# Kernel optimization log

Measured on AMD Instinct MI355X. Metric: run time of the kernel, lower is better.

Reference implementation:

```python
import jax, jax.numpy as jnp
import numpy as np

B, S, HID = 1, 2048, 4096
NH, NKV, HD = 32, 8, 128
GROUPS = NH // NKV
ROPE_THETA = 10000.0


def rotate_half(x):
    x1, x2 = jnp.split(x, 2, axis=-1)
    return jnp.concatenate([-x2, x1], axis=-1)


def rope_cos_sin(position_ids, head_dim, dtype):
    # inv_freq: [hd/2]; position_ids: [B, S]
    inv_freq = 1.0 / (ROPE_THETA ** (jnp.arange(0, head_dim, 2, dtype=jnp.float32) / head_dim))
    freqs = position_ids.astype(jnp.float32)[..., None] * inv_freq  # [B, S, hd/2]
    emb = jnp.concatenate([freqs, freqs], axis=-1)                  # [B, S, hd]
    return jnp.cos(emb).astype(dtype), jnp.sin(emb).astype(dtype)


def apply_rope(x, cos, sin):
    # x: [B, H, S, hd]; cos/sin: [B, S, hd] -> broadcast over heads
    return x * cos[:, None] + rotate_half(x) * sin[:, None]


def setup_inputs() -> dict:
    key = jax.random.key(0)
    ks = jax.random.split(key, 5)
    scale = 0.02
    return {
        "hidden_states": jax.random.normal(ks[0], (B, S, HID), dtype=jnp.float32),
        "wq": jax.random.normal(ks[1], (HID, NH * HD), dtype=jnp.float32) * scale,
        "wk": jax.random.normal(ks[2], (HID, NKV * HD), dtype=jnp.float32) * scale,
        "wv": jax.random.normal(ks[3], (HID, NKV * HD), dtype=jnp.float32) * scale,
        "wo": jax.random.normal(ks[4], (NH * HD, HID), dtype=jnp.float32) * scale,
        "position_ids": jnp.arange(S, dtype=jnp.int32)[None, :],
    }


def reference(hidden_states, wq, wk, wv, wo, position_ids):
    bsz, q_len, _ = hidden_states.shape
    # projections (nn.Linear, bias=False)
    q = (hidden_states @ wq).reshape(bsz, q_len, NH, HD).transpose(0, 2, 1, 3)   # [B,NH,S,hd]
    k = (hidden_states @ wk).reshape(bsz, q_len, NKV, HD).transpose(0, 2, 1, 3)  # [B,NKV,S,hd]
    v = (hidden_states @ wv).reshape(bsz, q_len, NKV, HD).transpose(0, 2, 1, 3)
    # RoPE applied to Q and K at global positions (prefill: no past cache)
    cos, sin = rope_cos_sin(position_ids, HD, q.dtype)
    q = apply_rope(q, cos, sin)
    k = apply_rope(k, cos, sin)
    # GQA: expand KV heads to query heads
    k_full = jnp.repeat(k, GROUPS, axis=1)  # [B,NH,S,hd]
    v_full = jnp.repeat(v, GROUPS, axis=1)
    # prefill flash attention == causal SDPA
    logits = jnp.einsum('bhqd,bhkd->bhqk', q, k_full) / jnp.sqrt(jnp.asarray(HD, q.dtype))
    causal = jnp.tril(jnp.ones((q_len, q_len), dtype=bool))
    neg = jnp.asarray(jnp.finfo(q.dtype).min, q.dtype)
    logits = jnp.where(causal[None, None], logits, neg)
    probs = jax.nn.softmax(logits, axis=-1)                     # [B,NH,S,S]
    attn = jnp.einsum('bhqk,bhkd->bhqd', probs, v_full)          # [B,NH,S,hd]
    attn_output = attn.transpose(0, 2, 1, 3).reshape(bsz, q_len, NH * HD) @ wo
    # chunked prefill eviction scores: causal attention probs accumulated over
    # all queries, aggregated per KV head group -> [B, NKV, kv_len]
    accumulated_scores = probs.sum(axis=2).reshape(bsz, NKV, GROUPS, q_len).sum(axis=2)
    return attn_output, accumulated_scores
```

## Files before the change

### kernel.cpp

```cpp
#include <hip/hip_runtime.h>
#include <hip/hip_bf16.h>
#include <cstdint>
#include <cstddef>

#define S_LEN 2048
#define HID_DIM 4096
#define NH 32
#define NKV 8
#define HD 128
#define LOG2E 1.4426950408889634f
#define SCALE 0.08838834764831845f

typedef __attribute__((ext_vector_type(8))) short bf16x8;
typedef __attribute__((ext_vector_type(4))) float f32x4;
typedef __attribute__((ext_vector_type(16))) float f32x16;
typedef __attribute__((ext_vector_type(4))) short short4v;
typedef __attribute__((ext_vector_type(4))) unsigned u32x4;

__device__ __forceinline__ short f2bf(float f) {
  union { float f; unsigned u; } v; v.f = f;
  return (short)((v.u + 0x7fffu + ((v.u >> 16) & 1u)) >> 16);
}
__device__ __forceinline__ float bf2f(short s) {
  union { unsigned u; float f; } v; v.u = ((unsigned)(unsigned short)s) << 16;
  return v.f;
}
__device__ __forceinline__ unsigned cvt_pk_bf16(float lo, float hi) {
  unsigned r;
  asm("v_cvt_pk_bf16_f32 %0, %1, %2" : "=v"(r) : "v"(lo), "v"(hi));
  return r;
}
__device__ __forceinline__ void gld_lds16(const void* g, void* l) {
  __builtin_amdgcn_global_load_lds((const __attribute__((address_space(1))) unsigned*)g,
                                   (__attribute__((address_space(3))) unsigned*)l, 16, 0, 0);
}

#define WAITVM8() asm volatile("s_waitcnt vmcnt(8)" ::: "memory")
#define WAITVM4() asm volatile("s_waitcnt vmcnt(4)" ::: "memory")
#define WAITVM0() asm volatile("s_waitcnt vmcnt(0)" ::: "memory")

__global__ void cvt_kernel(const float* __restrict__ in, short* __restrict__ out, int n) {
  int i = (blockIdx.x * 256 + threadIdx.x) * 4;
  if (i < n) {
    float4 f = *(const float4*)(in + i);
    short4v o = { f2bf(f.x), f2bf(f.y), f2bf(f.z), f2bf(f.w) };
    *(short4v*)(out + i) = o;
  }
}

__global__ void tconv_kernel(const float* __restrict__ in, short* __restrict__ out, int R, int C) {
  __shared__ float tile[32][33];
  int tr = blockIdx.y * 32, tc = blockIdx.x * 32;
  int tx = threadIdx.x & 31, ty = threadIdx.x >> 5;
#pragma unroll
  for (int i = 0; i < 32; i += 8)
    tile[ty + i][tx] = in[(size_t)(tr + ty + i) * C + tc + tx];
  __syncthreads();
#pragma unroll
  for (int i = 0; i < 32; i += 8)
    out[(size_t)(tc + ty + i) * R + tr + tx] = f2bf(tile[tx][ty + i]);
}

template<int MODE>
__global__ __launch_bounds__(256, 4) void gemm_bt_kernel(
    const short* __restrict__ A, const short* __restrict__ Bt,
    void* __restrict__ Cout, int M, int N, int K, int rchunk, int cchunk)
{
  __shared__ short As[2][128 * 32];
  __shared__ short Bs[2][128 * 32];
  const int tid = threadIdx.x;
  const int lane = tid & 63;
  const int w = tid >> 6;
  const int wm = w >> 1, wn = w & 1;
  const int xcd = blockIdx.x & 7;
  const int local = blockIdx.x >> 3;
  const int by = (xcd >> 2) * rchunk + (local % rchunk);
  const int bx = (xcd & 3) * cchunk + (local / rchunk);
  const int m0 = by * 128, n0 = bx * 128;

  auto stage = [&](int bb, int k0) {
#pragma unroll
    for (int rep = 0; rep < 2; rep++) {
      int c = rep * 256 + tid;
      int row = c >> 2, slot = c & 3;
      int gs = slot ^ (row & 3);
      gld_lds16(A + (size_t)(m0 + row) * K + k0 + gs * 8, &As[bb][c * 8]);
      gld_lds16(Bt + (size_t)(n0 + row) * K + k0 + gs * 8, &Bs[bb][c * 8]);
    }
  };

  f32x4 acc[4][4];
#pragma unroll
  for (int i = 0; i < 4; i++)
#pragma unroll
    for (int j = 0; j < 4; j++) acc[i][j] = (f32x4){0.f, 0.f, 0.f, 0.f};

  const int NT = K >> 5;
  stage(0, 0);
  for (int kt = 0; kt < NT; kt++) {
    const int b = kt & 1;
    if (kt + 1 < NT) { stage(b ^ 1, (kt + 1) << 5); WAITVM4(); }
    else             { WAITVM0(); }
    __builtin_amdgcn_s_barrier();

    bf16x8 af[4], bf[4];
#pragma unroll
    for (int ms = 0; ms < 4; ms++) {
      int row = wm * 64 + ms * 16 + (lane & 15);
      af[ms] = *(const bf16x8*)(&As[b][row * 32 + (((lane >> 4) ^ (row & 3)) << 3)]);
    }
#pragma unroll
    for (int ns = 0; ns < 4; ns++) {
      int row = wn * 64 + ns * 16 + (lane & 15);
      bf[ns] = *(const bf16x8*)(&Bs[b][row * 32 + (((lane >> 4) ^ (row & 3)) << 3)]);
    }
#pragma unroll
    for (int ms = 0; ms < 4; ms++)
#pragma unroll
      for (int ns = 0; ns < 4; ns++)
        acc[ms][ns] = __builtin_amdgcn_mfma_f32_16x16x32_bf16(af[ms], bf[ns], acc[ms][ns], 0, 0, 0);

    __builtin_amdgcn_s_barrier();
  }

#pragma unroll
  for (int ms = 0; ms < 4; ms++) {
    int mb = m0 + wm * 64 + ms * 16 + ((lane >> 4) << 2);
#pragma unroll
    for (int ns = 0; ns < 4; ns++) {
      int n = n0 + wn * 64 + ns * 16 + (lane & 15);
      if (MODE == 3) {
        short* o = (short*)Cout;
        if (n < NH * HD) {
          int head = n >> 7, d = n & 127;
#pragma unroll
          for (int r = 0; r < 4; r++)
            o[((size_t)head * M + (mb + r)) * HD + d] = f2bf(acc[ms][ns][r]);
        } else if (n < (NH + NKV) * HD) {
          int head = (n - NH * HD) >> 7, d = n & 127;
          short* ok = o + (size_t)NH * S_LEN * HD;
#pragma unroll
          for (int r = 0; r < 4; r++)
            ok[((size_t)head * M + (mb + r)) * HD + d] = f2bf(acc[ms][ns][r]);
        } else {
          int head = (n - (NH + NKV) * HD) >> 7, d = n & 127;
          short* ov = o + (size_t)(NH + NKV) * S_LEN * HD;
          short4v pk;
#pragma unroll
          for (int r = 0; r < 4; r++) pk[r] = f2bf(acc[ms][ns][r]);
          *(short4v*)(ov + ((size_t)head * HD + d) * M + mb) = pk;
        }
      } else {
        float* o = (float*)Cout;
#pragma unroll
        for (int r = 0; r < 4; r++)
          o[(size_t)(mb + r) * N + n] = acc[ms][ns][r];
      }
    }
  }
}

__global__ void rope_kernel(short* __restrict__ q, short* __restrict__ k,
                            const int* __restrict__ pos_ids) {
  const int s = blockIdx.x;
  const int hh = blockIdx.y * 4 + threadIdx.y;
  const int d = threadIdx.x;
  const float pos = (float)pos_ids[s];
  const float inv = __expf(-(float)d * 0.14391157f);
  float sn, c;
  __sincosf(pos * inv, &sn, &c);
  short* base = (hh < NH) ? (q + ((size_t)hh * S_LEN + s) * HD)
                          : (k + ((size_t)(hh - NH) * S_LEN + s) * HD);
  float x1 = bf2f(base[d]), x2 = bf2f(base[d + 64]);
  base[d] = f2bf(x1 * c - x2 * sn);
  base[d + 64] = f2bf(x2 * c + x1 * sn);
}

__global__ __launch_bounds__(256, 2) void attn_kernel(
    const short* __restrict__ Qr, const short* __restrict__ Kr, const short* __restrict__ Vt,
    short* __restrict__ attn_out, float* __restrict__ scores)
{
  __shared__ short Ks[2][64 * 128];
  __shared__ short Vs[2][128 * 64];
  __shared__ float cs[2048];

  const int tid = threadIdx.x;
  const int lane = tid & 63;
  const int w = tid >> 6;
  const int r = w & 1;
  const int kh = w >> 1;
  const int h2 = lane >> 5;
  const int l31 = lane & 31;
  const int xcd = blockIdx.x & 7;
  const int j = blockIdx.x >> 3;
  const int h = xcd * 4 + (j & 3);
  const int p = j >> 2;
  const int kvh = xcd;
  const float CS = SCALE * LOG2E;

  const short* KrB = Kr + (size_t)kvh * S_LEN * HD;
  const short* VtB = Vt + (size_t)kvh * HD * S_LEN;

  for (int i = tid; i < 2048; i += 256) cs[i] = 0.f;

  float* obuf = (float*)Ks;
  float* lbuf = (float*)Vs;
  float* rlbuf = lbuf + 64;

  auto stageK = [&](int bb, int t) {
    const int kb2 = t * 64;
#pragma unroll
    for (int rep = 0; rep < 4; rep++) {
      int c = rep * 256 + tid;
      int x = c >> 4, slot = c & 15;
      int key = (x & 0x33) | ((x & 4) << 1) | ((x & 8) >> 1);
      int gs = slot ^ (x & 7);
      gld_lds16(KrB + (size_t)(kb2 + key) * HD + gs * 8, &Ks[bb][c * 8]);
    }
  };
  auto stageV = [&](int bb, int t) {
    const int kb2 = t * 64;
#pragma unroll
    for (int rep = 0; rep < 4; rep++) {
      int c = rep * 256 + tid;
      int d = c >> 3, slot = c & 7;
      int gs = slot ^ (d & 7);
      gld_lds16(VtB + (size_t)d * S_LEN + kb2 + gs * 8, &Vs[bb][c * 8]);
    }
  };

  for (int sidx = 0; sidx < 2; sidx++) {
    const int qt = sidx ? p : (31 - p);
    const int nt = qt + 1;
    const int qbase = qt * 64 + r * 32;
    const int qglob = qbase + l31;
    const int qmaxw = qbase + 31;

    bf16x8 qf[8];
    {
      const short* qrow = Qr + ((size_t)h * S_LEN + qglob) * HD + h2 * 8;
#pragma unroll
      for (int kc = 0; kc < 8; kc++) qf[kc] = *(const bf16x8*)(qrow + kc * 16);
    }

    f32x16 oacc[4];
#pragma unroll
    for (int i = 0; i < 4; i++) oacc[i] = (f32x16)(0.f);
    float lsum = 0.f;

    stageK(0, 0); stageV(0, 0);
    for (int t = 0; t < nt; t++) {
      const int b = t & 1;
      const int kb = t * 64;
      if (t + 1 < nt) { stageK(b ^ 1, t + 1); stageV(b ^ 1, t + 1); WAITVM8(); }
      else            { WAITVM0(); }
      __builtin_amdgcn_s_barrier();

      if (kb <= qmaxw) {
        f32x16 sf = (f32x16)(0.f);
        const int x = kh * 32 + l31;
        __builtin_amdgcn_s_setprio(1);
#pragma unroll
        for (int kc = 0; kc < 8; kc++) {
          bf16x8 kf = *(const bf16x8*)(&Ks[b][x * 128 + (((kc * 2 + h2) ^ (x & 7)) << 3)]);
          sf = __builtin_amdgcn_mfma_f32_32x32x16_bf16(kf, qf[kc], sf, 0, 0, 0);
        }
        __builtin_amdgcn_s_setprio(0);

        float pv16[16];
        const bool diag = (kb + 63 > qbase);
#pragma unroll
        for (int a = 0; a < 4; a++)
#pragma unroll
          for (int cc = 0; cc < 4; cc++) {
            float pv = exp2f(sf[a * 4 + cc] * CS);
            if (diag) {
              int key = kb + kh * 32 + (a >> 1) * 16 + h2 * 8 + (a & 1) * 4 + cc;
              if (key > qglob) pv = 0.f;
            }
            pv16[a * 4 + cc] = pv;
            lsum += pv;
          }

        bf16x8 pa[2];
#pragma unroll
        for (int s = 0; s < 2; s++) {
          u32x4 pw;
          pw[0] = cvt_pk_bf16(pv16[8 * s + 0], pv16[8 * s + 1]);
          pw[1] = cvt_pk_bf16(pv16[8 * s + 2], pv16[8 * s + 3]);
          pw[2] = cvt_pk_bf16(pv16[8 * s + 4], pv16[8 * s + 5]);
          pw[3] = cvt_pk_bf16(pv16[8 * s + 6], pv16[8 * s + 7]);
          pa[s] = __builtin_bit_cast(bf16x8, pw);
        }

        __builtin_amdgcn_s_setprio(1);
#pragma unroll
        for (int s = 0; s < 2; s++) {
          const int g = kh * 2 + s;
#pragma unroll
          for (int db = 0; db < 4; db++) {
            int d = db * 32 + l31;
            bf16x8 vf = *(const bf16x8*)(&Vs[b][d * 64 + (((g * 2 + h2) ^ (d & 7)) << 3)]);
            oacc[db] = __builtin_amdgcn_mfma_f32_32x32x16_bf16(pa[s], vf, oacc[db], 0, 0, 0);
          }
        }
        __builtin_amdgcn_s_setprio(0);
      }
      __builtin_amdgcn_s_barrier();
    }

    lsum += __shfl_xor(lsum, 32);
    if (kh == 0) {
#pragma unroll
      for (int db = 0; db < 4; db++)
#pragma unroll
        for (int r16 = 0; r16 < 16; r16++) {
          int crow = (r16 & 3) + 8 * (r16 >> 2) + 4 * h2;
          obuf[(r * 32 + crow) * 128 + db * 32 + l31] = oacc[db][r16];
        }
      if (lane < 32) lbuf[r * 32 + l31] = lsum;
    }
    __builtin_amdgcn_s_barrier();

    if (kh == 1) {
      float ltot = lsum + lbuf[r * 32 + l31];
      float rlv = 1.f / ltot;
      float rl16[16];
#pragma unroll
      for (int r16 = 0; r16 < 16; r16++)
        rl16[r16] = __shfl(rlv, (r16 & 3) + 8 * (r16 >> 2) + 4 * h2);
#pragma unroll
      for (int db = 0; db < 4; db++) {
        int d = db * 32 + l31;
#pragma unroll
        for (int r16 = 0; r16 < 16; r16++) {
          int crow = (r16 & 3) + 8 * (r16 >> 2) + 4 * h2;
          float o = oacc[db][r16] + obuf[(r * 32 + crow) * 128 + d];
          attn_out[(size_t)(qbase + crow) * HID_DIM + h * HD + d] = f2bf(o * rl16[r16]);
        }
      }
      if (lane < 32) rlbuf[r * 32 + l31] = rlv;
    }
    __builtin_amdgcn_s_barrier();

    float rlv = rlbuf[r * 32 + l31];
    float rl16[16];
#pragma unroll
    for (int r16 = 0; r16 < 16; r16++)
      rl16[r16] = __shfl(rlv, (r16 & 3) + 8 * (r16 >> 2) + 4 * h2);
    __builtin_amdgcn_s_barrier();

    const int ntw = qmaxw / 64 + 1;
    for (int t = kh; t < ntw; t += 2) {
      const int kb = t * 64;
      f32x16 sg[2];
      sg[0] = (f32x16)(0.f); sg[1] = (f32x16)(0.f);
      __builtin_amdgcn_s_setprio(1);
#pragma unroll
      for (int kc = 0; kc < 8; kc++)
#pragma unroll
        for (int bl = 0; bl < 2; bl++) {
          bf16x8 kf = *(const bf16x8*)(KrB + (size_t)(kb + bl * 32 + l31) * HD + kc * 16 + h2 * 8);
          sg[bl] = __builtin_amdgcn_mfma_f32_32x32x16_bf16(qf[kc], kf, sg[bl], 0, 0, 0);
        }
      __builtin_amdgcn_s_setprio(0);

      const bool diag = (kb + 63 > qbase);
#pragma unroll
      for (int bl = 0; bl < 2; bl++) {
        int key = kb + bl * 32 + l31;
        float sum = 0.f;
#pragma unroll
        for (int r16 = 0; r16 < 16; r16++) {
          float pv = exp2f(sg[bl][r16] * CS) * rl16[r16];
          if (diag && key > qbase + (r16 & 3) + 8 * (r16 >> 2) + 4 * h2) pv = 0.f;
          sum += pv;
        }
        sum += __shfl_xor(sum, 32);
        if (lane < 32) atomicAdd(&cs[key], sum);
      }
    }
  }

  asm volatile("s_waitcnt lgkmcnt(0)" ::: "memory");
  __builtin_amdgcn_s_barrier();
  const int nk = (32 - p) * 64;
  for (int i = tid; i < nk; i += 256)
    atomicAdd(scores + (size_t)kvh * S_LEN + i, cs[i]);
}

extern "C" void kernel_launch(void* const* d_in, const int* in_sizes, int n_in,
                              void* d_out, int out_size, void* d_ws, size_t ws_size,
                              hipStream_t stream) {
  const float* hs = (const float*)d_in[0];
  const float* wq = (const float*)d_in[1];
  const float* wk = (const float*)d_in[2];
  const float* wv = (const float*)d_in[3];
  const float* wo = (const float*)d_in[4];
  const int* pos = (const int*)d_in[5];
  float* out = (float*)d_out;

  char* ws = (char*)d_ws;
  const size_t off_hs   = 0;
  const size_t off_wqT  = off_hs   + (size_t)S_LEN * HID_DIM * 2;
  const size_t off_wkT  = off_wqT  + (size_t)HID_DIM * HID_DIM * 2;
  const size_t off_wvT  = off_wkT  + (size_t)1024 * HID_DIM * 2;
  const size_t off_woT  = off_wvT  + (size_t)1024 * HID_DIM * 2;
  const size_t off_Qr   = off_woT  + (size_t)HID_DIM * HID_DIM * 2;
  const size_t off_Kr   = off_Qr   + (size_t)NH * S_LEN * HD * 2;
  const size_t off_Vt   = off_Kr   + (size_t)NKV * S_LEN * HD * 2;
  const size_t off_attn = off_Vt   + (size_t)NKV * HD * S_LEN * 2;

  short* hsb  = (short*)(ws + off_hs);
  short* wqT  = (short*)(ws + off_wqT);
  short* wkT  = (short*)(ws + off_wkT);
  short* wvT  = (short*)(ws + off_wvT);
  short* woT  = (short*)(ws + off_woT);
  short* Qr   = (short*)(ws + off_Qr);
  short* Kr   = (short*)(ws + off_Kr);
  short* Vt   = (short*)(ws + off_Vt);
  short* attb = (short*)(ws + off_attn);

  cvt_kernel<<<dim3((S_LEN * HID_DIM) / 1024), 256, 0, stream>>>(hs, hsb, S_LEN * HID_DIM);
  tconv_kernel<<<dim3(128, 128), 256, 0, stream>>>(wq, wqT, HID_DIM, HID_DIM);
  tconv_kernel<<<dim3(32, 128), 256, 0, stream>>>(wk, wkT, HID_DIM, 1024);
  tconv_kernel<<<dim3(32, 128), 256, 0, stream>>>(wv, wvT, HID_DIM, 1024);
  tconv_kernel<<<dim3(128, 128), 256, 0, stream>>>(wo, woT, HID_DIM, HID_DIM);

  gemm_bt_kernel<3><<<768, 256, 0, stream>>>(hsb, wqT, Qr, S_LEN, 6144, HID_DIM, 8, 12);

  rope_kernel<<<dim3(S_LEN, 10), dim3(64, 4), 0, stream>>>(Qr, Kr, pos);

  hipMemsetAsync(out + (size_t)S_LEN * HID_DIM, 0, (size_t)NKV * S_LEN * sizeof(float), stream);
  attn_kernel<<<512, 256, 0, stream>>>(Qr, Kr, Vt, attb, out + (size_t)S_LEN * HID_DIM);

  gemm_bt_kernel<2><<<512, 256, 0, stream>>>(attb, woT, out, S_LEN, HID_DIM, HID_DIM, 8, 8);
}
```

Before: 391.9 us.

## Split attention into one q-tile per block, single-buffer V, drop LDS score buffer

```diff
diff --git a/kernel.cpp b/kernel.cpp
--- a/kernel.cpp
+++ b/kernel.cpp
@@ -35,7 +35,6 @@
                                    (__attribute__((address_space(3))) unsigned*)l, 16, 0, 0);
 }
 
-#define WAITVM8() asm volatile("s_waitcnt vmcnt(8)" ::: "memory")
 #define WAITVM4() asm volatile("s_waitcnt vmcnt(4)" ::: "memory")
 #define WAITVM0() asm volatile("s_waitcnt vmcnt(0)" ::: "memory")
 
@@ -176,13 +175,13 @@
   base[d + 64] = f2bf(x2 * c + x1 * sn);
 }
 
-__global__ __launch_bounds__(256, 2) void attn_kernel(
+__global__ __launch_bounds__(256, 3) void attn_kernel(
     const short* __restrict__ Qr, const short* __restrict__ Kr, const short* __restrict__ Vt,
     short* __restrict__ attn_out, float* __restrict__ scores)
 {
   __shared__ short Ks[2][64 * 128];
-  __shared__ short Vs[2][128 * 64];
-  __shared__ float cs[2048];
+  __shared__ short Vs[128 * 64];
+  __shared__ float lbuf[128];
 
   const int tid = threadIdx.x;
   const int lane = tid & 63;
@@ -194,18 +193,18 @@
   const int xcd = blockIdx.x & 7;
   const int j = blockIdx.x >> 3;
   const int h = xcd * 4 + (j & 3);
-  const int p = j >> 2;
+  const int qt = 31 - (j >> 2);
   const int kvh = xcd;
   const float CS = SCALE * LOG2E;
 
   const short* KrB = Kr + (size_t)kvh * S_LEN * HD;
   const short* VtB = Vt + (size_t)kvh * HD * S_LEN;
 
-  for (int i = tid; i < 2048; i += 256) cs[i] = 0.f;
+  const int nt = qt + 1;
+  const int qbase = qt * 64 + r * 32;
+  const int qglob = qbase + l31;
 
   float* obuf = (float*)Ks;
-  float* lbuf = (float*)Vs;
-  float* rlbuf = lbuf + 64;
 
   auto stageK = [&](int bb, int t) {
     const int kb2 = t * 64;
@@ -218,175 +217,165 @@
       gld_lds16(KrB + (size_t)(kb2 + key) * HD + gs * 8, &Ks[bb][c * 8]);
     }
   };
-  auto stageV = [&](int bb, int t) {
+  auto stageV = [&](int t) {
     const int kb2 = t * 64;
 #pragma unroll
     for (int rep = 0; rep < 4; rep++) {
       int c = rep * 256 + tid;
       int d = c >> 3, slot = c & 7;
       int gs = slot ^ (d & 7);
-      gld_lds16(VtB + (size_t)d * S_LEN + kb2 + gs * 8, &Vs[bb][c * 8]);
+      gld_lds16(VtB + (size_t)d * S_LEN + kb2 + gs * 8, &Vs[c * 8]);
     }
   };
 
-  for (int sidx = 0; sidx < 2; sidx++) {
-    const int qt = sidx ? p : (31 - p);
-    const int nt = qt + 1;
-    const int qbase = qt * 64 + r * 32;
-    const int qglob = qbase + l31;
-    const int qmaxw = qbase + 31;
-
-    bf16x8 qf[8];
-    {
-      const short* qrow = Qr + ((size_t)h * S_LEN + qglob) * HD + h2 * 8;
-#pragma unroll
-      for (int kc = 0; kc < 8; kc++) qf[kc] = *(const bf16x8*)(qrow + kc * 16);
-    }
-
-    f32x16 oacc[4];
-#pragma unroll
-    for (int i = 0; i < 4; i++) oacc[i] = (f32x16)(0.f);
-    float lsum = 0.f;
-
-    stageK(0, 0); stageV(0, 0);
-    for (int t = 0; t < nt; t++) {
-      const int b = t & 1;
-      const int kb = t * 64;
-      if (t + 1 < nt) { stageK(b ^ 1, t + 1); stageV(b ^ 1, t + 1); WAITVM8(); }
-      else            { WAITVM0(); }
-      __builtin_amdgcn_s_barrier();
-
-      if (kb <= qmaxw) {
-        f32x16 sf = (f32x16)(0.f);
-        const int x = kh * 32 + l31;
-        __builtin_amdgcn_s_setprio(1);
-#pragma unroll
-        for (int kc = 0; kc < 8; kc++) {
-          bf16x8 kf = *(const bf16x8*)(&Ks[b][x * 128 + (((kc * 2 + h2) ^ (x & 7)) << 3)]);
-          sf = __builtin_amdgcn_mfma_f32_32x32x16_bf16(kf, qf[kc], sf, 0, 0, 0);
+  bf16x8 qf[8];
+  {
+    const short* qrow = Qr + ((size_t)h * S_LEN + qglob) * HD + h2 * 8;
+#pragma unroll
+    for (int kc = 0; kc < 8; kc++) qf[kc] = *(const bf16x8*)(qrow + kc * 16);
+  }
+
+  f32x16 oacc[4];
+#pragma unroll
+  for (int i = 0; i < 4; i++) oacc[i] = (f32x16)(0.f);
+  float lsum = 0.f;
+
+  stageK(0, 0);
+  for (int t = 0; t < nt; t++) {
+    const int b = t & 1;
+    const int kb = t * 64;
+    WAITVM0();
+    __builtin_amdgcn_s_barrier();
+
+    stageV(t);
+    if (t + 1 < nt) stageK(b ^ 1, t + 1);
+
+    f32x16 sf = (f32x16)(0.f);
+    const int x = kh * 32 + l31;
+    __builtin_amdgcn_s_setprio(1);
+#pragma unroll
+    for (int kc = 0; kc < 8; kc++) {
+      bf16x8 kf = *(const bf16x8*)(&Ks[b][x * 128 + (((kc * 2 + h2) ^ (x & 7)) << 3)]);
+      sf = __builtin_amdgcn_mfma_f32_32x32x16_bf16(kf, qf[kc], sf, 0, 0, 0);
+    }
+    __builtin_amdgcn_s_setprio(0);
+
+    float pv16[16];
+    const bool diag = (kb + 63 > qbase);
+#pragma unroll
+    for (int a = 0; a < 4; a++)
+#pragma unroll
+      for (int cc = 0; cc < 4; cc++) {
+        float pv = exp2f(sf[a * 4 + cc] * CS);
+        if (diag) {
+          int key = kb + kh * 32 + (a >> 1) * 16 + h2 * 8 + (a & 1) * 4 + cc;
+          if (key > qglob) pv = 0.f;
         }
-        __builtin_amdgcn_s_setprio(0);
-
-        float pv16[16];
-        const bool diag = (kb + 63 > qbase);
-#pragma unroll
-        for (int a = 0; a < 4; a++)
-#pragma unroll
-          for (int cc = 0; cc < 4; cc++) {
-            float pv = exp2f(sf[a * 4 + cc] * CS);
-            if (diag) {
-              int key = kb + kh * 32 + (a >> 1) * 16 + h2 * 8 + (a & 1) * 4 + cc;
-              if (key > qglob) pv = 0.f;
-            }
-            pv16[a * 4 + cc] = pv;
-            lsum += pv;
-          }
-
-        bf16x8 pa[2];
-#pragma unroll
-        for (int s = 0; s < 2; s++) {
-          u32x4 pw;
-          pw[0] = cvt_pk_bf16(pv16[8 * s + 0], pv16[8 * s + 1]);
-          pw[1] = cvt_pk_bf16(pv16[8 * s + 2], pv16[8 * s + 3]);
-          pw[2] = cvt_pk_bf16(pv16[8 * s + 4], pv16[8 * s + 5]);
-          pw[3] = cvt_pk_bf16(pv16[8 * s + 6], pv16[8 * s + 7]);
-          pa[s] = __builtin_bit_cast(bf16x8, pw);
-        }
-
-        __builtin_amdgcn_s_setprio(1);
-#pragma unroll
-        for (int s = 0; s < 2; s++) {
-          const int g = kh * 2 + s;
-#pragma unroll
-          for (int db = 0; db < 4; db++) {
-            int d = db * 32 + l31;
-            bf16x8 vf = *(const bf16x8*)(&Vs[b][d * 64 + (((g * 2 + h2) ^ (d & 7)) << 3)]);
-            oacc[db] = __builtin_amdgcn_mfma_f32_32x32x16_bf16(pa[s], vf, oacc[db], 0, 0, 0);
-          }
-        }
-        __builtin_amdgcn_s_setprio(0);
-      }
-      __builtin_amdgcn_s_barrier();
-    }
-
-    lsum += __shfl_xor(lsum, 32);
-    if (kh == 0) {
-#pragma unroll
-      for (int db = 0; db < 4; db++)
-#pragma unroll
-        for (int r16 = 0; r16 < 16; r16++) {
-          int crow = (r16 & 3) + 8 * (r16 >> 2) + 4 * h2;
-          obuf[(r * 32 + crow) * 128 + db * 32 + l31] = oacc[db][r16];
-        }
-      if (lane < 32) lbuf[r * 32 + l31] = lsum;
-    }
+        pv16[a * 4 + cc] = pv;
+        lsum += pv;
+      }
+
+    bf16x8 pa[2];
+#pragma unroll
+    for (int s = 0; s < 2; s++) {
+      u32x4 pw;
+      pw[0] = cvt_pk_bf16(pv16[8 * s + 0], pv16[8 * s + 1]);
+      pw[1] = cvt_pk_bf16(pv16[8 * s + 2], pv16[8 * s + 3]);
+      pw[2] = cvt_pk_bf16(pv16[8 * s + 4], pv16[8 * s + 5]);
+      pw[3] = cvt_pk_bf16(pv16[8 * s + 6], pv16[8 * s + 7]);
+      pa[s] = __builtin_bit_cast(bf16x8, pw);
+    }
+
+    if (t + 1 < nt) WAITVM4();
+    else           WAITVM0();
     __builtin_amdgcn_s_barrier();
 
-    if (kh == 1) {
-      float ltot = lsum + lbuf[r * 32 + l31];
-      float rlv = 1.f / ltot;
-      float rl16[16];
-#pragma unroll
-      for (int r16 = 0; r16 < 16; r16++)
-        rl16[r16] = __shfl(rlv, (r16 & 3) + 8 * (r16 >> 2) + 4 * h2);
+    __builtin_amdgcn_s_setprio(1);
+#pragma unroll
+    for (int s = 0; s < 2; s++) {
+      const int g = kh * 2 + s;
 #pragma unroll
       for (int db = 0; db < 4; db++) {
         int d = db * 32 + l31;
-#pragma unroll
-        for (int r16 = 0; r16 < 16; r16++) {
-          int crow = (r16 & 3) + 8 * (r16 >> 2) + 4 * h2;
-          float o = oacc[db][r16] + obuf[(r * 32 + crow) * 128 + d];
-          attn_out[(size_t)(qbase + crow) * HID_DIM + h * HD + d] = f2bf(o * rl16[r16]);
-        }
-      }
-      if (lane < 32) rlbuf[r * 32 + l31] = rlv;
-    }
-    __builtin_amdgcn_s_barrier();
-
-    float rlv = rlbuf[r * 32 + l31];
+        bf16x8 vf = *(const bf16x8*)(&Vs[d * 64 + (((g * 2 + h2) ^ (d & 7)) << 3)]);
+        oacc[db] = __builtin_amdgcn_mfma_f32_32x32x16_bf16(pa[s], vf, oacc[db], 0, 0, 0);
+      }
+    }
+    __builtin_amdgcn_s_setprio(0);
+  }
+
+  __builtin_amdgcn_s_barrier();
+
+  lsum += __shfl_xor(lsum, 32);
+  if (kh == 0) {
+#pragma unroll
+    for (int db = 0; db < 4; db++)
+#pragma unroll
+      for (int r16 = 0; r16 < 16; r16++) {
+        int crow = (r16 & 3) + 8 * (r16 >> 2) + 4 * h2;
+        obuf[(r * 32 + crow) * 128 + db * 32 + l31] = oacc[db][r16];
+      }
+    if (lane < 32) lbuf[r * 32 + l31] = lsum;
+  }
+  __builtin_amdgcn_s_barrier();
+
+  if (kh == 1) {
+    float ltot = lsum + lbuf[r * 32 + l31];
+    float rlv = 1.f / ltot;
     float rl16[16];
 #pragma unroll
     for (int r16 = 0; r16 < 16; r16++)
       rl16[r16] = __shfl(rlv, (r16 & 3) + 8 * (r16 >> 2) + 4 * h2);
-    __builtin_amdgcn_s_barrier();
-
-    const int ntw = qmaxw / 64 + 1;
-    for (int t = kh; t < ntw; t += 2) {
-      const int kb = t * 64;
-      f32x16 sg[2];
-      sg[0] = (f32x16)(0.f); sg[1] = (f32x16)(0.f);
-      __builtin_amdgcn_s_setprio(1);
-#pragma unroll
-      for (int kc = 0; kc < 8; kc++)
-#pragma unroll
-        for (int bl = 0; bl < 2; bl++) {
-          bf16x8 kf = *(const bf16x8*)(KrB + (size_t)(kb + bl * 32 + l31) * HD + kc * 16 + h2 * 8);
-          sg[bl] = __builtin_amdgcn_mfma_f32_32x32x16_bf16(qf[kc], kf, sg[bl], 0, 0, 0);
-        }
-      __builtin_amdgcn_s_setprio(0);
-
-      const bool diag = (kb + 63 > qbase);
+#pragma unroll
+    for (int db = 0; db < 4; db++) {
+      int d = db * 32 + l31;
+#pragma unroll
+      for (int r16 = 0; r16 < 16; r16++) {
+        int crow = (r16 & 3) + 8 * (r16 >> 2) + 4 * h2;
+        float o = oacc[db][r16] + obuf[(r * 32 + crow) * 128 + d];
+        attn_out[(size_t)(qbase + crow) * HID_DIM + h * HD + d] = f2bf(o * rl16[r16]);
+      }
+    }
+    if (lane < 32) lbuf[64 + r * 32 + l31] = rlv;
+  }
+  __builtin_amdgcn_s_barrier();
+
+  float rlv = lbuf[64 + r * 32 + l31];
+  float rl16[16];
+#pragma unroll
+  for (int r16 = 0; r16 < 16; r16++)
+    rl16[r16] = __shfl(rlv, (r16 & 3) + 8 * (r16 >> 2) + 4 * h2);
+
+  float* sc = scores + (size_t)kvh * S_LEN;
+  for (int t = kh; t < nt; t += 2) {
+    const int kb = t * 64;
+    f32x16 sg[2];
+    sg[0] = (f32x16)(0.f); sg[1] = (f32x16)(0.f);
+    __builtin_amdgcn_s_setprio(1);
+#pragma unroll
+    for (int kc = 0; kc < 8; kc++)
 #pragma unroll
       for (int bl = 0; bl < 2; bl++) {
-        int key = kb + bl * 32 + l31;
-        float sum = 0.f;
-#pragma unroll
-        for (int r16 = 0; r16 < 16; r16++) {
-          float pv = exp2f(sg[bl][r16] * CS) * rl16[r16];
-          if (diag && key > qbase + (r16 & 3) + 8 * (r16 >> 2) + 4 * h2) pv = 0.f;
-          sum += pv;
-        }
-        sum += __shfl_xor(sum, 32);
-        if (lane < 32) atomicAdd(&cs[key], sum);
-      }
-    }
-  }
-
-  asm volatile("s_waitcnt lgkmcnt(0)" ::: "memory");
-  __builtin_amdgcn_s_barrier();
-  const int nk = (32 - p) * 64;
-  for (int i = tid; i < nk; i += 256)
-    atomicAdd(scores + (size_t)kvh * S_LEN + i, cs[i]);
+        bf16x8 kf = *(const bf16x8*)(KrB + (size_t)(kb + bl * 32 + l31) * HD + kc * 16 + h2 * 8);
+        sg[bl] = __builtin_amdgcn_mfma_f32_32x32x16_bf16(qf[kc], kf, sg[bl], 0, 0, 0);
+      }
+    __builtin_amdgcn_s_setprio(0);
+
+    const bool diag = (kb + 63 > qbase);
+#pragma unroll
+    for (int bl = 0; bl < 2; bl++) {
+      int key = kb + bl * 32 + l31;
+      float sum = 0.f;
+#pragma unroll
+      for (int r16 = 0; r16 < 16; r16++) {
+        float pv = exp2f(sg[bl][r16] * CS) * rl16[r16];
+        if (diag && key > qbase + (r16 & 3) + 8 * (r16 >> 2) + 4 * h2) pv = 0.f;
+        sum += pv;
+      }
+      sum += __shfl_xor(sum, 32);
+      if (lane < 32) atomicAdd(&sc[key], sum);
+    }
+  }
 }
 
 extern "C" void kernel_launch(void* const* d_in, const int* in_sizes, int n_in,
@@ -432,7 +421,7 @@
   rope_kernel<<<dim3(S_LEN, 10), dim3(64, 4), 0, stream>>>(Qr, Kr, pos);
 
   hipMemsetAsync(out + (size_t)S_LEN * HID_DIM, 0, (size_t)NKV * S_LEN * sizeof(float), stream);
-  attn_kernel<<<512, 256, 0, stream>>>(Qr, Kr, Vt, attb, out + (size_t)S_LEN * HID_DIM);
+  attn_kernel<<<1024, 256, 0, stream>>>(Qr, Kr, Vt, attb, out + (size_t)S_LEN * HID_DIM);
 
   gemm_bt_kernel<2><<<512, 256, 0, stream>>>(attb, woT, out, S_LEN, HID_DIM, HID_DIM, 8, 8);
 }
```

Result: no change. 399.1 us (+1.8%).
